# Kernel optimization log

Hardware: AMD Instinct MI355X
Metric: run time of the kernel (lower is better)

Reference implementation:

```python
import jax, jax.numpy as jnp
import numpy as np

N, E, E3, DIM = 25000, 50000, 40000, 64


def setup_inputs() -> dict:
    key = jax.random.key(0)
    ks = jax.random.split(key, 16)
    def g(k, shape, scale=0.1):
        return jax.random.normal(k, shape, jnp.float32) * scale
    return {
        "x": jax.random.normal(ks[0], (N, 8), jnp.float32),
        "edge_attr": jax.random.uniform(ks[1], (E, 19), dtype=jnp.float32),
        "edge_attr3": jax.random.uniform(ks[2], (E3, 8), dtype=jnp.float32),
        "edge_index": jax.random.randint(ks[3], (2, E), 0, N),
        "edge_index3": jax.random.randint(ks[4], (2, E3), 0, N),
        "W_node": g(ks[5], (8, DIM)), "b_node": jnp.zeros((DIM,), jnp.float32),
        "W_ea": g(ks[6], (19, 12)), "b_ea": jnp.zeros((12,), jnp.float32),
        "W_e1": g(ks[7], (12, 128)), "b_e1": jnp.zeros((128,), jnp.float32),
        "W_e2": g(ks[8], (128, DIM * DIM), 0.01), "b_e2": jnp.zeros((DIM * DIM,), jnp.float32),
        "conv_bias": jnp.zeros((DIM,), jnp.float32),
        "W_ih": g(ks[9], (3 * DIM, DIM)), "b_ih": jnp.zeros((3 * DIM,), jnp.float32),
        "W_hh": g(ks[10], (3 * DIM, DIM)), "b_hh": jnp.zeros((3 * DIM,), jnp.float32),
        "W_l1": g(ks[11], (DIM + 8, 128)), "b_l1": jnp.zeros((128,), jnp.float32),
        "W_l2": g(ks[12], (128, 1)), "b_l2": jnp.zeros((1,), jnp.float32),
    }


def _forward(x, edge_attr, edge_attr3,
             W_node, b_node, W_ea, b_ea, W_e1, b_e1, W_e2, b_e2, conv_bias,
             W_ih, b_ih, W_hh, b_hh, W_l1, b_l1, W_l2, b_l2,
             edge_index, edge_index3):
    dim = W_node.shape[1]
    n = x.shape[0]
    out = jax.nn.relu(x @ W_node + b_node)                      # [N, dim]
    ea = jax.nn.relu(edge_attr @ W_ea + b_ea)                   # [E, 12]
    # edge MLP -> per-edge dim x dim weight matrices (same for all 3 conv calls)
    Wedge = (jax.nn.relu(ea @ W_e1 + b_e1) @ W_e2 + b_e2).reshape(-1, dim, dim)  # [E, dim, dim]
    src, dst = edge_index[0], edge_index[1]
    ones = jnp.ones((src.shape[0],), x.dtype)
    cnt = jnp.maximum(jax.ops.segment_sum(ones, dst, num_segments=n), 1.0)  # [N]
    h = out
    for _ in range(3):
        msg = jnp.einsum('ed,edf->ef', out[src], Wedge)                     # per-edge GEMV
        agg = jax.ops.segment_sum(msg, dst, num_segments=n) / cnt[:, None]  # scatter-mean
        m = jax.nn.relu(agg + conv_bias)
        # single-step GRU (PyTorch gate order: r, z, n)
        gi = m @ W_ih.T + b_ih
        gh = h @ W_hh.T + b_hh
        ir, iz, inn = jnp.split(gi, 3, axis=-1)
        hr, hz, hn = jnp.split(gh, 3, axis=-1)
        r = jax.nn.sigmoid(ir + hr)
        z = jax.nn.sigmoid(iz + hz)
        ng = jnp.tanh(inn + r * hn)
        h = (1.0 - z) * ng + z * h
        out = h
    pair = (out[edge_index3[0]] + out[edge_index3[1]]) * 0.5    # mean over the 2 endpoints
    yhat = jnp.concatenate([pair, edge_attr3], axis=1)          # [E3, dim+8]
    yhat = jax.nn.relu(yhat @ W_l1 + b_l1) @ W_l2 + b_l2        # [E3, 1]
    return yhat[:, 0]


def reference(x, edge_attr, edge_attr3, edge_index, edge_index3,
              W_node, b_node, W_ea, b_ea, W_e1, b_e1, W_e2, b_e2, conv_bias,
              W_ih, b_ih, W_hh, b_hh, W_l1, b_l1, W_l2, b_l2):
    return _forward(x, edge_attr, edge_attr3,
                    W_node, b_node, W_ea, b_ea, W_e1, b_e1, W_e2, b_e2, conv_bias,
                    W_ih, b_ih, W_hh, b_hh, W_l1, b_l1, W_l2, b_l2,
                    edge_index, edge_index3)
```

## Files before the change

kernel.cpp:

```cpp
#include <hip/hip_runtime.h>

typedef unsigned short u16;
typedef unsigned int u32;
typedef __attribute__((ext_vector_type(8))) short short8v;
typedef __attribute__((ext_vector_type(4))) float float4v;

__device__ __forceinline__ float sigm(float x) { return 1.0f / (1.0f + __expf(-x)); }
__device__ __forceinline__ u16 f2bf(float f) {
  u32 u = __float_as_uint(f);
  u32 r = (u + 0x7fffu + ((u >> 16) & 1u)) >> 16;
  return (u16)r;
}
__device__ __forceinline__ float bf2f(u16 w) { return __uint_as_float(((u32)w) << 16); }

__global__ void k_cnt(const int* __restrict__ dst, int* __restrict__ cnt, int E) {
  int e = blockIdx.x * blockDim.x + threadIdx.x;
  if (e < E) atomicAdd(&cnt[dst[e]], 1);
}

__global__ void k_scan1(const int* __restrict__ cnt, int* __restrict__ bsum, int N) {
  __shared__ int ws[4];
  int t = threadIdx.x;
  int i = blockIdx.x * 256 + t;
  int v = (i < N) ? cnt[i] : 0;
  int s = v;
  for (int off = 1; off < 64; off <<= 1) s += __shfl_xor(s, off);
  int wid = t >> 6, lane = t & 63;
  if (lane == 0) ws[wid] = s;
  __syncthreads();
  if (t == 0) bsum[blockIdx.x] = ws[0] + ws[1] + ws[2] + ws[3];
}

__global__ void k_scan2(int* __restrict__ bsum, int* __restrict__ row, int nb, int N) {
  __shared__ int s[256];
  int t = threadIdx.x;
  if (t < nb) s[t] = bsum[t];
  __syncthreads();
  if (t == 0) {
    int run = 0;
    for (int i = 0; i < nb; ++i) { int x = s[i]; s[i] = run; run += x; }
    row[N] = run;
  }
  __syncthreads();
  if (t < nb) bsum[t] = s[t];
}

__global__ void k_scan3(const int* __restrict__ cnt, const int* __restrict__ bsum,
                        int* __restrict__ row, int* __restrict__ cursor, int N) {
  __shared__ int ws[4];
  int t = threadIdx.x;
  int i = blockIdx.x * 256 + t;
  int v = (i < N) ? cnt[i] : 0;
  int lane = t & 63, wid = t >> 6;
  int incl = v;
  for (int off = 1; off < 64; off <<= 1) {
    int u = __shfl_up(incl, off);
    if (lane >= off) incl += u;
  }
  if (lane == 63) ws[wid] = incl;
  __syncthreads();
  int woff = bsum[blockIdx.x];
  for (int w = 0; w < wid; ++w) woff += ws[w];
  int excl = woff + incl - v;
  if (i < N) { row[i] = excl; cursor[i] = excl; }
}

__global__ void k_pos(const int* __restrict__ dst, int* __restrict__ cursor,
                      int* __restrict__ pos, int E) {
  int e = blockIdx.x * blockDim.x + threadIdx.x;
  if (e < E) pos[e] = atomicAdd(&cursor[dst[e]], 1);
}

__global__ __launch_bounds__(256) void k_edge_mlp(
    const float* __restrict__ ea_in, const float* __restrict__ Wea,
    const float* __restrict__ bea, const float* __restrict__ We1,
    const float* __restrict__ be1, u16* __restrict__ Ahi, int E) {
  __shared__ float att[2][19];
  __shared__ float ea[2][12];
  int half = threadIdx.x >> 7;
  int t = threadIdx.x & 127;
  int e = blockIdx.x * 2 + half;
  bool real = (e < E);
  int ee = real ? e : E - 1;
  if (t < 19) att[half][t] = ea_in[(size_t)ee * 19 + t];
  __syncthreads();
  if (t < 12) {
    float a = bea[t];
#pragma unroll
    for (int k = 0; k < 19; ++k) a += att[half][k] * Wea[k * 12 + t];
    ea[half][t] = fmaxf(a, 0.0f);
  }
  __syncthreads();
  float a = be1[t];
#pragma unroll
  for (int j = 0; j < 12; ++j) a += ea[half][j] * We1[j * 128 + t];
  if (real) Ahi[(size_t)e * 128 + t] = f2bf(fmaxf(a, 0.0f));
}

__global__ void k_prep_all(
    const float* __restrict__ x, const float* __restrict__ Wn,
    const float* __restrict__ bn, float* __restrict__ h, int N, int nbNode,
    const float* __restrict__ W2, u16* __restrict__ Bph, int nbPack,
    const float* __restrict__ Wih, const float* __restrict__ Whh,
    u16* __restrict__ WpI, u16* __restrict__ WpH, int nbWtf,
    const float* __restrict__ Wl1, u16* __restrict__ Wp1) {
  int b = blockIdx.x;
  if (b < nbNode) {
    int tid = b * 256 + threadIdx.x;
    if (tid >= N * 64) return;
    int n = tid >> 6, f = tid & 63;
    float acc = bn[f];
    for (int k = 0; k < 8; ++k) acc += x[(size_t)n * 8 + k] * Wn[k * 64 + f];
    h[tid] = fmaxf(acc, 0.0f);
  } else if (b < nbNode + nbPack) {
    int tid = (b - nbNode) * 256 + threadIdx.x;
    if (tid >= 128 * 4096) return;
    int j = tid & 7;
    int lane = (tid >> 3) & 63;
    int nt = (tid >> 9) & 3;
    int ks = (tid >> 11) & 3;
    int d = tid >> 13;
    int c = lane & 15, q = lane >> 4;
    int k = ks * 32 + q * 8 + j;
    int n = d * 64 + nt * 16 + c;
    Bph[tid] = f2bf(W2[(size_t)k * 4096 + n]);
  } else if (b < nbNode + nbPack + nbWtf) {
    int tid = (b - nbNode - nbPack) * 256 + threadIdx.x;
    if (tid >= 2 * 12288) return;
    int w = tid / 12288;
    int r = tid - w * 12288;
    int jj = r & 7;
    int lane = (r >> 3) & 63;
    int t = r >> 9;
    int nt = t % 12, ks = t / 12;
    int c = lane & 15, q = lane >> 4;
    int j = nt * 16 + c;
    int k = ks * 32 + q * 8 + jj;
    const float* W = w ? Whh : Wih;
    u16* Wp = w ? WpH : WpI;
    Wp[r] = f2bf(W[j * 64 + k]);
  } else {
    int tid = (b - nbNode - nbPack - nbWtf) * 256 + threadIdx.x;
    if (tid >= 3 * 8 * 64 * 8) return;
    int j = tid & 7;
    int lane = (tid >> 3) & 63;
    int nt = (tid >> 9) & 7;
    int ks = tid >> 12;
    int c = lane & 15, q = lane >> 4;
    int k = ks * 32 + q * 8 + j;
    int n = nt * 16 + c;
    Wp1[tid] = f2bf((k < 72) ? Wl1[k * 128 + n] : 0.0f);
  }
}

__global__ __launch_bounds__(256, 2) void k_conv_fused(
    const u16* __restrict__ Ahi, const u16* __restrict__ Bph,
    const float* __restrict__ b2, const float* __restrict__ h,
    const int* __restrict__ src, const int* __restrict__ pos,
    u16* __restrict__ msgh, int E) {
  __shared__ __align__(16) u16 sB[2][8192];
  __shared__ __align__(16) float hsT[64 * 132];
  __shared__ __align__(16) u16 sb2h[4096];
  int m0 = blockIdx.x * 128;
  int tid = threadIdx.x;
  int wave = tid >> 6, lane = tid & 63;
  int mw = wave >> 1, fw = wave & 1;
  int c = lane & 15, q = lane >> 4;

  auto stageB = [&](int d, int b) {
    const u16* gp = Bph + (size_t)d * 8192 + wave * 2048 + lane * 8;
    u16* lp = &sB[b][wave * 2048];
#pragma unroll
    for (int i = 0; i < 4; ++i)
      __builtin_amdgcn_global_load_lds(
          (const __attribute__((address_space(1))) unsigned int*)(gp + i * 512),
          (__attribute__((address_space(3))) unsigned int*)(lp + i * 512), 16, 0, 0);
  };

  stageB(0, 0);

  short8v afr[4][4];
#pragma unroll
  for (int mt = 0; mt < 4; ++mt) {
    int gr = m0 + mw * 64 + mt * 16 + c;
    if (gr >= E) gr = E - 1;
    const u16* ap = Ahi + (size_t)gr * 128 + q * 8;
#pragma unroll
    for (int ks = 0; ks < 4; ++ks) afr[mt][ks] = *(const short8v*)(ap + ks * 32);
  }

#pragma unroll
  for (int p = 0; p < 8; ++p) {
    int slot = p * 256 + tid;
    int r = slot >> 4, s = slot & 15;
    int ge = m0 + r;
    if (ge >= E) ge = E - 1;
    int sn = src[ge];
    float4 v = *(const float4*)(h + (size_t)sn * 64 + s * 4);
    hsT[(s * 4 + 0) * 132 + r] = v.x;
    hsT[(s * 4 + 1) * 132 + r] = v.y;
    hsT[(s * 4 + 2) * 132 + r] = v.z;
    hsT[(s * 4 + 3) * 132 + r] = v.w;
  }
  {
    int t16 = tid * 16;
#pragma unroll
    for (int u = 0; u < 4; ++u) {
      float4 v = *(const float4*)(b2 + t16 + u * 4);
      sb2h[t16 + u * 4 + 0] = f2bf(v.x);
      sb2h[t16 + u * 4 + 1] = f2bf(v.y);
      sb2h[t16 + u * 4 + 2] = f2bf(v.z);
      sb2h[t16 + u * 4 + 3] = f2bf(v.w);
    }
  }
  __syncthreads();

  float msg[4][2][4];
#pragma unroll
  for (int mt = 0; mt < 4; ++mt)
#pragma unroll
    for (int nt = 0; nt < 2; ++nt)
#pragma unroll
      for (int r = 0; r < 4; ++r) msg[mt][nt][r] = 0.0f;

  int cur = 0;
  for (int dl = 0; dl < 64; ++dl) {
    if (dl < 63) stageB(dl + 1, cur ^ 1);
    float b2v0 = bf2f(sb2h[dl * 64 + fw * 32 + c]);
    float b2v1 = bf2f(sb2h[dl * 64 + fw * 32 + 16 + c]);
    float4v acc[4][2];
#pragma unroll
    for (int mt = 0; mt < 4; ++mt)
#pragma unroll
      for (int nt = 0; nt < 2; ++nt) acc[mt][nt] = (float4v){0.f, 0.f, 0.f, 0.f};
    __builtin_amdgcn_s_setprio(1);
#pragma unroll
    for (int ks = 0; ks < 4; ++ks) {
      short8v b0 = *(const short8v*)(&sB[cur][ks * 2048 + fw * 1024 + lane * 8]);
      short8v b1 = *(const short8v*)(&sB[cur][ks * 2048 + fw * 1024 + 512 + lane * 8]);
#pragma unroll
      for (int mt = 0; mt < 4; ++mt) {
        acc[mt][0] = __builtin_amdgcn_mfma_f32_16x16x32_bf16(afr[mt][ks], b0, acc[mt][0], 0, 0, 0);
        acc[mt][1] = __builtin_amdgcn_mfma_f32_16x16x32_bf16(afr[mt][ks], b1, acc[mt][1], 0, 0, 0);
      }
    }
    __builtin_amdgcn_s_setprio(0);
#pragma unroll
    for (int mt = 0; mt < 4; ++mt) {
      float4 hd4 = *(const float4*)(&hsT[dl * 132 + mw * 64 + mt * 16 + q * 4]);
      float hd[4] = {hd4.x, hd4.y, hd4.z, hd4.w};
#pragma unroll
      for (int r = 0; r < 4; ++r) {
        msg[mt][0][r] += hd[r] * (acc[mt][0][r] + b2v0);
        msg[mt][1][r] += hd[r] * (acc[mt][1][r] + b2v1);
      }
    }
    __syncthreads();
    cur ^= 1;
  }

#pragma unroll
  for (int mt = 0; mt < 4; ++mt) {
#pragma unroll
    for (int r = 0; r < 4; ++r) {
      int e = m0 + mw * 64 + mt * 16 + q * 4 + r;
      if (e < E) {
        int pe = pos[e];
        u16* mp = msgh + (size_t)pe * 64 + fw * 32 + c;
        mp[0] = f2bf(msg[mt][0][r]);
        mp[16] = f2bf(msg[mt][1][r]);
      }
    }
  }
}

__global__ __launch_bounds__(256, 2) void k_gru_mfma(
    const u16* __restrict__ msgh, const int* __restrict__ row,
    const float* __restrict__ cb, const u16* __restrict__ WpI,
    const u16* __restrict__ WpH, const float* __restrict__ bih,
    const float* __restrict__ bhh, const float* __restrict__ hin,
    float* __restrict__ hout, int N) {
  __shared__ __align__(16) u16 sM[64 * 72];
  __shared__ __align__(16) u16 sH[64 * 72];
  __shared__ __align__(16) float sHf[64 * 68];
  __shared__ int sRow[65];
  int n0 = blockIdx.x * 64;
  int tid = threadIdx.x;
  if (tid < 65) {
    int idx = n0 + tid;
    sRow[tid] = row[(idx <= N) ? idx : N];
  }
  __syncthreads();
  {
    int nl = tid >> 4, fq = tid & 15;
    float4 cbv = *(const float4*)(cb + fq * 4);
#pragma unroll
    for (int pass = 0; pass < 4; ++pass) {
      int n = pass * 16 + nl;
      int gn = n0 + n;
      bool real = (gn < N);
      int b0 = sRow[n], b1 = sRow[n + 1];
      if (!real) b1 = b0;
      float4 av = {0.f, 0.f, 0.f, 0.f};
      for (int j = b0; j < b1; ++j) {
        ushort4 mv = *(const ushort4*)(msgh + (size_t)j * 64 + fq * 4);
        av.x += bf2f(mv.x); av.y += bf2f(mv.y);
        av.z += bf2f(mv.z); av.w += bf2f(mv.w);
      }
      float cf = fmaxf((float)(b1 - b0), 1.0f);
      int hgn = real ? gn : N - 1;
      float4 hv = *(const float4*)(hin + (size_t)hgn * 64 + fq * 4);
      float m0v = fmaxf(av.x / cf + cbv.x, 0.0f);
      float m1v = fmaxf(av.y / cf + cbv.y, 0.0f);
      float m2v = fmaxf(av.z / cf + cbv.z, 0.0f);
      float m3v = fmaxf(av.w / cf + cbv.w, 0.0f);
      ushort4 mu; mu.x = f2bf(m0v); mu.y = f2bf(m1v); mu.z = f2bf(m2v); mu.w = f2bf(m3v);
      ushort4 hu; hu.x = f2bf(hv.x); hu.y = f2bf(hv.y); hu.z = f2bf(hv.z); hu.w = f2bf(hv.w);
      *(ushort4*)(&sM[n * 72 + fq * 4]) = mu;
      *(ushort4*)(&sH[n * 72 + fq * 4]) = hu;
      *(float4*)(&sHf[n * 68 + fq * 4]) = hv;
    }
  }
  __syncthreads();
  int wave = tid >> 6, lane = tid & 63;
  int c = lane & 15, q = lane >> 4;
  short8v am[2], ah[2];
#pragma unroll
  for (int ks = 0; ks < 2; ++ks) {
    am[ks] = *(const short8v*)(&sM[(wave * 16 + c) * 72 + ks * 32 + q * 8]);
    ah[ks] = *(const short8v*)(&sH[(wave * 16 + c) * 72 + ks * 32 + q * 8]);
  }
  float4v accRZ[8], accN[4], accHN[4];
#pragma unroll
  for (int i = 0; i < 8; ++i) accRZ[i] = (float4v){0.f, 0.f, 0.f, 0.f};
#pragma unroll
  for (int i = 0; i < 4; ++i) {
    accN[i] = (float4v){0.f, 0.f, 0.f, 0.f};
    accHN[i] = (float4v){0.f, 0.f, 0.f, 0.f};
  }
#pragma unroll
  for (int ks = 0; ks < 2; ++ks) {
#pragma unroll
    for (int nt = 0; nt < 8; ++nt) {
      short8v bI = *(const short8v*)(WpI + ((size_t)(ks * 12 + nt) * 64 + lane) * 8);
      short8v bH = *(const short8v*)(WpH + ((size_t)(ks * 12 + nt) * 64 + lane) * 8);
      accRZ[nt] = __builtin_amdgcn_mfma_f32_16x16x32_bf16(am[ks], bI, accRZ[nt], 0, 0, 0);
      accRZ[nt] = __builtin_amdgcn_mfma_f32_16x16x32_bf16(ah[ks], bH, accRZ[nt], 0, 0, 0);
    }
#pragma unroll
    for (int nt = 0; nt < 4; ++nt) {
      short8v bI = *(const short8v*)(WpI + ((size_t)(ks * 12 + 8 + nt) * 64 + lane) * 8);
      short8v bH = *(const short8v*)(WpH + ((size_t)(ks * 12 + 8 + nt) * 64 + lane) * 8);
      accN[nt] = __builtin_amdgcn_mfma_f32_16x16x32_bf16(am[ks], bI, accN[nt], 0, 0, 0);
      accHN[nt] = __builtin_amdgcn_mfma_f32_16x16x32_bf16(ah[ks], bH, accHN[nt], 0, 0, 0);
    }
  }
#pragma unroll
  for (int nt = 0; nt < 4; ++nt) {
    int f = nt * 16 + c;
    float brz_r = bih[f] + bhh[f];
    float brz_z = bih[64 + f] + bhh[64 + f];
    float bin = bih[128 + f];
    float bhn = bhh[128 + f];
#pragma unroll
    for (int r = 0; r < 4; ++r) {
      int nl = wave * 16 + q * 4 + r;
      int gn = n0 + nl;
      float rr = sigm(accRZ[nt][r] + brz_r);
      float zz = sigm(accRZ[nt + 4][r] + brz_z);
      float ng = tanhf(accN[nt][r] + bin + rr * (accHN[nt][r] + bhn));
      float hv = sHf[nl * 68 + f];
      if (gn < N) hout[(size_t)gn * 64 + f] = (1.0f - zz) * ng + zz * hv;
    }
  }
}

__global__ __launch_bounds__(256) void k_final_mfma(
    const float* __restrict__ h, const float* __restrict__ ea3,
    const int* __restrict__ idx3, const u16* __restrict__ Wp1,
    const float* __restrict__ bl1, const float* __restrict__ Wl2,
    const float* __restrict__ bl2, float* __restrict__ out, int E3) {
  __shared__ __align__(16) u16 sF[64 * 104];
  int e0 = blockIdx.x * 64;
  int tid = threadIdx.x;
  {
    int er = tid >> 2;
    int part = tid & 3;
    int ge = e0 + er;
    int gc = (ge < E3) ? ge : E3 - 1;
    int a = idx3[gc], b = idx3[E3 + gc];
    const float* pa = h + (size_t)a * 64 + part * 16;
    const float* pb = h + (size_t)b * 64 + part * 16;
#pragma unroll
    for (int u = 0; u < 4; ++u) {
      float4 va = *(const float4*)(pa + u * 4);
      float4 vb = *(const float4*)(pb + u * 4);
      ushort4 mu;
      mu.x = f2bf(0.5f * (va.x + vb.x));
      mu.y = f2bf(0.5f * (va.y + vb.y));
      mu.z = f2bf(0.5f * (va.z + vb.z));
      mu.w = f2bf(0.5f * (va.w + vb.w));
      *(ushort4*)(&sF[er * 104 + part * 16 + u * 4]) = mu;
    }
    if (part == 0) {
      float4 e0v = *(const float4*)(ea3 + (size_t)gc * 8);
      float4 e1v = *(const float4*)(ea3 + (size_t)gc * 8 + 4);
      ushort4 u0, u1;
      u0.x = f2bf(e0v.x); u0.y = f2bf(e0v.y); u0.z = f2bf(e0v.z); u0.w = f2bf(e0v.w);
      u1.x = f2bf(e1v.x); u1.y = f2bf(e1v.y); u1.z = f2bf(e1v.z); u1.w = f2bf(e1v.w);
      *(ushort4*)(&sF[er * 104 + 64]) = u0;
      *(ushort4*)(&sF[er * 104 + 68]) = u1;
    } else {
      ushort4 z = {0, 0, 0, 0};
      *(ushort4*)(&sF[er * 104 + 72 + (part - 1) * 8]) = z;
      *(ushort4*)(&sF[er * 104 + 76 + (part - 1) * 8]) = z;
    }
  }
  __syncthreads();
  int wave = tid >> 6, lane = tid & 63;
  int c = lane & 15, q = lane >> 4;
  float4v acc[8];
#pragma unroll
  for (int nt = 0; nt < 8; ++nt) acc[nt] = (float4v){0.f, 0.f, 0.f, 0.f};
#pragma unroll
  for (int ks = 0; ks < 3; ++ks) {
    short8v af = *(const short8v*)(&sF[(wave * 16 + c) * 104 + ks * 32 + q * 8]);
#pragma unroll
    for (int nt = 0; nt < 8; ++nt) {
      short8v bf = *(const short8v*)(Wp1 + ((size_t)(ks * 8 + nt) * 64 + lane) * 8);
      acc[nt] = __builtin_amdgcn_mfma_f32_16x16x32_bf16(af, bf, acc[nt], 0, 0, 0);
    }
  }
  float v[4] = {0.f, 0.f, 0.f, 0.f};
#pragma unroll
  for (int nt = 0; nt < 8; ++nt) {
    int n = nt * 16 + c;
    float b1 = bl1[n];
    float w2 = Wl2[n];
#pragma unroll
    for (int r = 0; r < 4; ++r) v[r] += fmaxf(acc[nt][r] + b1, 0.0f) * w2;
  }
#pragma unroll
  for (int off = 1; off < 16; off <<= 1) {
#pragma unroll
    for (int r = 0; r < 4; ++r) v[r] += __shfl_xor(v[r], off);
  }
  if (c == 0) {
    float b2v = bl2[0];
#pragma unroll
    for (int r = 0; r < 4; ++r) {
      int e = e0 + wave * 16 + q * 4 + r;
      if (e < E3) out[e] = v[r] + b2v;
    }
  }
}

extern "C" void kernel_launch(void* const* d_in, const int* in_sizes, int n_in,
                              void* d_out, int out_size, void* d_ws, size_t ws_size,
                              hipStream_t stream) {
  const float* x          = (const float*)d_in[0];
  const float* edge_attr  = (const float*)d_in[1];
  const float* edge_attr3 = (const float*)d_in[2];
  const int*   edge_index = (const int*)d_in[3];
  const int*   edge_index3= (const int*)d_in[4];
  const float* W_node = (const float*)d_in[5];
  const float* b_node = (const float*)d_in[6];
  const float* W_ea   = (const float*)d_in[7];
  const float* b_ea   = (const float*)d_in[8];
  const float* W_e1   = (const float*)d_in[9];
  const float* b_e1   = (const float*)d_in[10];
  const float* W_e2   = (const float*)d_in[11];
  const float* b_e2   = (const float*)d_in[12];
  const float* conv_bias = (const float*)d_in[13];
  const float* W_ih   = (const float*)d_in[14];
  const float* b_ih   = (const float*)d_in[15];
  const float* W_hh   = (const float*)d_in[16];
  const float* b_hh   = (const float*)d_in[17];
  const float* W_l1   = (const float*)d_in[18];
  const float* b_l1   = (const float*)d_in[19];
  const float* W_l2   = (const float*)d_in[20];
  const float* b_l2   = (const float*)d_in[21];

  int N  = in_sizes[0] / 8;
  int E  = in_sizes[1] / 19;
  int E3 = in_sizes[2] / 8;

  char* p = (char*)d_ws;
  auto carve = [&](size_t bytes) -> void* {
    char* q = p;
    p += (bytes + 255) & ~(size_t)255;
    return (void*)q;
  };
  float* hA    = (float*)carve((size_t)N * 64 * 4);
  float* hB    = (float*)carve((size_t)N * 64 * 4);
  u16*   msgh  = (u16*)carve((size_t)E * 64 * 2);
  int*   cnt   = (int*)carve((size_t)N * 4);
  int*   row   = (int*)carve((size_t)(N + 1) * 4);
  int*   cursor= (int*)carve((size_t)N * 4);
  int*   pos   = (int*)carve((size_t)E * 4);
  int*   bsum  = (int*)carve(256 * 4);
  u16*   Ahi   = (u16*)carve((size_t)E * 128 * 2);
  u16*   Bph   = (u16*)carve((size_t)128 * 4096 * 2);
  u16*   WpI   = (u16*)carve(12288 * 2);
  u16*   WpH   = (u16*)carve(12288 * 2);
  u16*   Wp1   = (u16*)carve(12288 * 2);

  const int* src = edge_index;
  const int* dst = edge_index + E;

  int nb = (N + 255) / 256;
  hipMemsetAsync(cnt, 0, (size_t)N * 4, stream);
  k_cnt<<<(E + 255) / 256, 256, 0, stream>>>(dst, cnt, E);
  k_scan1<<<nb, 256, 0, stream>>>(cnt, bsum, N);
  k_scan2<<<1, 256, 0, stream>>>(bsum, row, nb, N);
  k_scan3<<<nb, 256, 0, stream>>>(cnt, bsum, row, cursor, N);
  k_pos<<<(E + 255) / 256, 256, 0, stream>>>(dst, cursor, pos, E);

  k_edge_mlp<<<(E + 1) / 2, 256, 0, stream>>>(edge_attr, W_ea, b_ea, W_e1, b_e1, Ahi, E);
  int nbNode = ((size_t)N * 64 + 255) / 256;
  int nbPack = (128 * 4096 + 255) / 256;
  int nbWtf  = (2 * 12288 + 255) / 256;
  int nbWl1  = (12288 + 255) / 256;
  k_prep_all<<<nbNode + nbPack + nbWtf + nbWl1, 256, 0, stream>>>(
      x, W_node, b_node, hA, N, nbNode, W_e2, Bph, nbPack,
      W_ih, W_hh, WpI, WpH, nbWtf, W_l1, Wp1);

  float* hcur = hA;
  float* hnxt = hB;
  int gconv = (E + 127) / 128;
  int ngru = (N + 63) / 64;
  for (int it = 0; it < 3; ++it) {
    k_conv_fused<<<gconv, 256, 0, stream>>>(Ahi, Bph, b_e2, hcur, src, pos, msgh, E);
    k_gru_mfma<<<ngru, 256, 0, stream>>>(msgh, row, conv_bias, WpI, WpH,
                                         b_ih, b_hh, hcur, hnxt, N);
    float* tmp = hcur; hcur = hnxt; hnxt = tmp;
  }
  k_final_mfma<<<(E3 + 63) / 64, 256, 0, stream>>>(hcur, edge_attr3, edge_index3, Wp1,
                                                   b_l1, W_l2, b_l2, (float*)d_out, E3);
}
```

Baseline: 398.0 us.

## Split conv kernel across output-feature halves, swizzle LDS, fold edge MLP into prep

The fused conv kernel now runs a 2D grid where blockIdx.y picks one 32-wide half of the output features. This halves the per-block LDS B tile, the accumulator registers and the bias staging, and raises launch bounds to 3 blocks per CU for more occupancy. The cost is that A fragments and the gathered h rows are loaded twice, once per half. The transposed h tile drops its padding in favour of an XOR swizzle to avoid LDS bank conflicts. The separate edge-MLP kernel is merged into k_prep_all as one thread per edge with vectorized bf16 stores, removing a launch.

Result: slower. 508.1 us (+27.7%).

```diff
diff --git a/kernel.cpp b/kernel.cpp
--- a/kernel.cpp
+++ b/kernel.cpp
@@ -71,39 +71,16 @@
   if (e < E) pos[e] = atomicAdd(&cursor[dst[e]], 1);
 }
 
-__global__ __launch_bounds__(256) void k_edge_mlp(
-    const float* __restrict__ ea_in, const float* __restrict__ Wea,
-    const float* __restrict__ bea, const float* __restrict__ We1,
-    const float* __restrict__ be1, u16* __restrict__ Ahi, int E) {
-  __shared__ float att[2][19];
-  __shared__ float ea[2][12];
-  int half = threadIdx.x >> 7;
-  int t = threadIdx.x & 127;
-  int e = blockIdx.x * 2 + half;
-  bool real = (e < E);
-  int ee = real ? e : E - 1;
-  if (t < 19) att[half][t] = ea_in[(size_t)ee * 19 + t];
-  __syncthreads();
-  if (t < 12) {
-    float a = bea[t];
-#pragma unroll
-    for (int k = 0; k < 19; ++k) a += att[half][k] * Wea[k * 12 + t];
-    ea[half][t] = fmaxf(a, 0.0f);
-  }
-  __syncthreads();
-  float a = be1[t];
-#pragma unroll
-  for (int j = 0; j < 12; ++j) a += ea[half][j] * We1[j * 128 + t];
-  if (real) Ahi[(size_t)e * 128 + t] = f2bf(fmaxf(a, 0.0f));
-}
-
 __global__ void k_prep_all(
     const float* __restrict__ x, const float* __restrict__ Wn,
     const float* __restrict__ bn, float* __restrict__ h, int N, int nbNode,
     const float* __restrict__ W2, u16* __restrict__ Bph, int nbPack,
     const float* __restrict__ Wih, const float* __restrict__ Whh,
     u16* __restrict__ WpI, u16* __restrict__ WpH, int nbWtf,
-    const float* __restrict__ Wl1, u16* __restrict__ Wp1) {
+    const float* __restrict__ Wl1, u16* __restrict__ Wp1, int nbWl1,
+    const float* __restrict__ ea_in, const float* __restrict__ Wea,
+    const float* __restrict__ bea, const float* __restrict__ We1,
+    const float* __restrict__ be1, u16* __restrict__ Ahi, int E) {
   int b = blockIdx.x;
   if (b < nbNode) {
     int tid = b * 256 + threadIdx.x;
@@ -139,7 +116,7 @@
     const float* W = w ? Whh : Wih;
     u16* Wp = w ? WpH : WpI;
     Wp[r] = f2bf(W[j * 64 + k]);
-  } else {
+  } else if (b < nbNode + nbPack + nbWtf + nbWl1) {
     int tid = (b - nbNode - nbPack - nbWtf) * 256 + threadIdx.x;
     if (tid >= 3 * 8 * 64 * 8) return;
     int j = tid & 7;
@@ -150,28 +127,57 @@
     int k = ks * 32 + q * 8 + j;
     int n = nt * 16 + c;
     Wp1[tid] = f2bf((k < 72) ? Wl1[k * 128 + n] : 0.0f);
-  }
-}
-
-__global__ __launch_bounds__(256, 2) void k_conv_fused(
+  } else {
+    int e = (b - nbNode - nbPack - nbWtf - nbWl1) * 256 + threadIdx.x;
+    if (e >= E) return;
+    float att[19];
+#pragma unroll
+    for (int k = 0; k < 19; ++k) att[k] = ea_in[(size_t)e * 19 + k];
+    float ea[12];
+#pragma unroll
+    for (int t = 0; t < 12; ++t) {
+      float a = bea[t];
+#pragma unroll
+      for (int k = 0; k < 19; ++k) a += att[k] * Wea[k * 12 + t];
+      ea[t] = fmaxf(a, 0.0f);
+    }
+#pragma unroll
+    for (int ch = 0; ch < 16; ++ch) {
+      float acc[8];
+#pragma unroll
+      for (int i = 0; i < 8; ++i) acc[i] = be1[ch * 8 + i];
+#pragma unroll
+      for (int j = 0; j < 12; ++j)
+#pragma unroll
+        for (int i = 0; i < 8; ++i) acc[i] += ea[j] * We1[j * 128 + ch * 8 + i];
+      short8v ov;
+#pragma unroll
+      for (int i = 0; i < 8; ++i) ov[i] = (short)f2bf(fmaxf(acc[i], 0.0f));
+      *(short8v*)(Ahi + (size_t)e * 128 + ch * 8) = ov;
+    }
+  }
+}
+
+__global__ __launch_bounds__(256, 3) void k_conv_fused(
     const u16* __restrict__ Ahi, const u16* __restrict__ Bph,
     const float* __restrict__ b2, const float* __restrict__ h,
     const int* __restrict__ src, const int* __restrict__ pos,
     u16* __restrict__ msgh, int E) {
-  __shared__ __align__(16) u16 sB[2][8192];
-  __shared__ __align__(16) float hsT[64 * 132];
-  __shared__ __align__(16) u16 sb2h[4096];
+  __shared__ __align__(16) u16 sB[2][4096];
+  __shared__ __align__(16) float hsT[64 * 128];
+  __shared__ __align__(16) u16 sb2h[2048];
   int m0 = blockIdx.x * 128;
+  int y = blockIdx.y;
   int tid = threadIdx.x;
   int wave = tid >> 6, lane = tid & 63;
   int mw = wave >> 1, fw = wave & 1;
   int c = lane & 15, q = lane >> 4;
 
   auto stageB = [&](int d, int b) {
-    const u16* gp = Bph + (size_t)d * 8192 + wave * 2048 + lane * 8;
-    u16* lp = &sB[b][wave * 2048];
-#pragma unroll
-    for (int i = 0; i < 4; ++i)
+    const u16* gp = Bph + (size_t)d * 8192 + wave * 2048 + y * 1024 + lane * 8;
+    u16* lp = &sB[b][wave * 1024];
+#pragma unroll
+    for (int i = 0; i < 2; ++i)
       __builtin_amdgcn_global_load_lds(
           (const __attribute__((address_space(1))) unsigned int*)(gp + i * 512),
           (__attribute__((address_space(3))) unsigned int*)(lp + i * 512), 16, 0, 0);
@@ -197,63 +203,51 @@
     if (ge >= E) ge = E - 1;
     int sn = src[ge];
     float4 v = *(const float4*)(h + (size_t)sn * 64 + s * 4);
-    hsT[(s * 4 + 0) * 132 + r] = v.x;
-    hsT[(s * 4 + 1) * 132 + r] = v.y;
-    hsT[(s * 4 + 2) * 132 + r] = v.z;
-    hsT[(s * 4 + 3) * 132 + r] = v.w;
+    int col = r ^ ((s & 7) << 2);
+    hsT[(s * 4 + 0) * 128 + col] = v.x;
+    hsT[(s * 4 + 1) * 128 + col] = v.y;
+    hsT[(s * 4 + 2) * 128 + col] = v.z;
+    hsT[(s * 4 + 3) * 128 + col] = v.w;
   }
   {
-    int t16 = tid * 16;
-#pragma unroll
-    for (int u = 0; u < 4; ++u) {
-      float4 v = *(const float4*)(b2 + t16 + u * 4);
-      sb2h[t16 + u * 4 + 0] = f2bf(v.x);
-      sb2h[t16 + u * 4 + 1] = f2bf(v.y);
-      sb2h[t16 + u * 4 + 2] = f2bf(v.z);
-      sb2h[t16 + u * 4 + 3] = f2bf(v.w);
-    }
-  }
-  __syncthreads();
-
-  float msg[4][2][4];
+#pragma unroll
+    for (int i = 0; i < 8; ++i) {
+      int idx = tid * 8 + i;
+      int dl = idx >> 5, fl = idx & 31;
+      sb2h[idx] = f2bf(b2[(size_t)dl * 64 + y * 32 + fl]);
+    }
+  }
+  __syncthreads();
+
+  float msg[4][4];
 #pragma unroll
   for (int mt = 0; mt < 4; ++mt)
 #pragma unroll
-    for (int nt = 0; nt < 2; ++nt)
-#pragma unroll
-      for (int r = 0; r < 4; ++r) msg[mt][nt][r] = 0.0f;
+    for (int r = 0; r < 4; ++r) msg[mt][r] = 0.0f;
 
   int cur = 0;
   for (int dl = 0; dl < 64; ++dl) {
     if (dl < 63) stageB(dl + 1, cur ^ 1);
-    float b2v0 = bf2f(sb2h[dl * 64 + fw * 32 + c]);
-    float b2v1 = bf2f(sb2h[dl * 64 + fw * 32 + 16 + c]);
-    float4v acc[4][2];
-#pragma unroll
-    for (int mt = 0; mt < 4; ++mt)
-#pragma unroll
-      for (int nt = 0; nt < 2; ++nt) acc[mt][nt] = (float4v){0.f, 0.f, 0.f, 0.f};
+    float b2v = bf2f(sb2h[dl * 32 + fw * 16 + c]);
+    float4v acc[4];
+#pragma unroll
+    for (int mt = 0; mt < 4; ++mt) acc[mt] = (float4v){0.f, 0.f, 0.f, 0.f};
     __builtin_amdgcn_s_setprio(1);
 #pragma unroll
     for (int ks = 0; ks < 4; ++ks) {
-      short8v b0 = *(const short8v*)(&sB[cur][ks * 2048 + fw * 1024 + lane * 8]);
-      short8v b1 = *(const short8v*)(&sB[cur][ks * 2048 + fw * 1024 + 512 + lane * 8]);
-#pragma unroll
-      for (int mt = 0; mt < 4; ++mt) {
-        acc[mt][0] = __builtin_amdgcn_mfma_f32_16x16x32_bf16(afr[mt][ks], b0, acc[mt][0], 0, 0, 0);
-        acc[mt][1] = __builtin_amdgcn_mfma_f32_16x16x32_bf16(afr[mt][ks], b1, acc[mt][1], 0, 0, 0);
-      }
+      short8v bfrag = *(const short8v*)(&sB[cur][ks * 1024 + fw * 512 + lane * 8]);
+#pragma unroll
+      for (int mt = 0; mt < 4; ++mt)
+        acc[mt] = __builtin_amdgcn_mfma_f32_16x16x32_bf16(afr[mt][ks], bfrag, acc[mt], 0, 0, 0);
     }
     __builtin_amdgcn_s_setprio(0);
+    int swz = ((dl >> 2) & 7) << 2;
 #pragma unroll
     for (int mt = 0; mt < 4; ++mt) {
-      float4 hd4 = *(const float4*)(&hsT[dl * 132 + mw * 64 + mt * 16 + q * 4]);
+      float4 hd4 = *(const float4*)(&hsT[dl * 128 + ((mw * 64 + mt * 16 + q * 4) ^ swz)]);
       float hd[4] = {hd4.x, hd4.y, hd4.z, hd4.w};
 #pragma unroll
-      for (int r = 0; r < 4; ++r) {
-        msg[mt][0][r] += hd[r] * (acc[mt][0][r] + b2v0);
-        msg[mt][1][r] += hd[r] * (acc[mt][1][r] + b2v1);
-      }
+      for (int r = 0; r < 4; ++r) msg[mt][r] += hd[r] * (acc[mt][r] + b2v);
     }
     __syncthreads();
     cur ^= 1;
@@ -266,9 +260,7 @@
       int e = m0 + mw * 64 + mt * 16 + q * 4 + r;
       if (e < E) {
         int pe = pos[e];
-        u16* mp = msgh + (size_t)pe * 64 + fw * 32 + c;
-        mp[0] = f2bf(msg[mt][0][r]);
-        mp[16] = f2bf(msg[mt][1][r]);
+        msgh[(size_t)pe * 64 + y * 32 + fw * 16 + c] = f2bf(msg[mt][r]);
       }
     }
   }
@@ -516,18 +508,19 @@
   k_scan3<<<nb, 256, 0, stream>>>(cnt, bsum, row, cursor, N);
   k_pos<<<(E + 255) / 256, 256, 0, stream>>>(dst, cursor, pos, E);
 
-  k_edge_mlp<<<(E + 1) / 2, 256, 0, stream>>>(edge_attr, W_ea, b_ea, W_e1, b_e1, Ahi, E);
   int nbNode = ((size_t)N * 64 + 255) / 256;
   int nbPack = (128 * 4096 + 255) / 256;
   int nbWtf  = (2 * 12288 + 255) / 256;
   int nbWl1  = (12288 + 255) / 256;
-  k_prep_all<<<nbNode + nbPack + nbWtf + nbWl1, 256, 0, stream>>>(
+  int nbEdge = (E + 255) / 256;
+  k_prep_all<<<nbNode + nbPack + nbWtf + nbWl1 + nbEdge, 256, 0, stream>>>(
       x, W_node, b_node, hA, N, nbNode, W_e2, Bph, nbPack,
-      W_ih, W_hh, WpI, WpH, nbWtf, W_l1, Wp1);
+      W_ih, W_hh, WpI, WpH, nbWtf, W_l1, Wp1, nbWl1,
+      edge_attr, W_ea, b_ea, W_e1, b_e1, Ahi, E);
 
   float* hcur = hA;
   float* hnxt = hB;
-  int gconv = (E + 127) / 128;
+  dim3 gconv((E + 127) / 128, 2);
   int ngru = (N + 63) / 64;
   for (int it = 0; it < 3; ++it) {
     k_conv_fused<<<gconv, 256, 0, stream>>>(Ahi, Bph, b_e2, hcur, src, pos, msgh, E);
```
